# Performance work log

Hardware: AMD Instinct MI355X
Metric: run time of the kernel (lower is better)

## Reference

```python
import jax, jax.numpy as jnp
import numpy as np

CAPACITY = 0.5


def setup_inputs() -> dict:
    key = jax.random.key(0)
    ks = jax.random.split(key, 7)
    b, s, d, h = 4, 8192, 1024, 4096
    sc_r = 1.0 / np.sqrt(d)
    sc_1 = 1.0 / np.sqrt(d)
    sc_2 = 1.0 / np.sqrt(h)
    return {
        "x": jax.random.normal(ks[0], (b, s, d), dtype=jnp.float32),
        # router Linear(d, 1)
        "w_r": jax.random.uniform(ks[1], (d, 1), jnp.float32, -sc_r, sc_r),
        "b_r": jax.random.uniform(ks[2], (1,), jnp.float32, -sc_r, sc_r),
        # token-wise MLP block: Linear(d, h) -> GELU -> Linear(h, d)
        "W1": jax.random.uniform(ks[3], (d, h), jnp.float32, -sc_1, sc_1),
        "b1": jax.random.uniform(ks[4], (h,), jnp.float32, -sc_1, sc_1),
        "W2": jax.random.uniform(ks[5], (h, d), jnp.float32, -sc_2, sc_2),
        "b2": jax.random.uniform(ks[6], (d,), jnp.float32, -sc_2, sc_2),
    }


def reference(x, w_r, b_r, W1, b1, W2, b2):
    b, s, d = x.shape
    k = int(CAPACITY * s)
    # router: Linear(d,1) -> squeeze -> [b, s]
    weights = (jnp.einsum("bsd,do->bso", x, w_r) + b_r).squeeze(-1)
    # k-th largest per batch row (topk sorted descending, take last)
    top_vals, _ = jax.lax.top_k(weights, k)  # [b, k]
    threshold = top_vals[:, -1]              # [b]
    selected = weights > threshold[:, None]  # strict >, ties excluded (as in torch code)
    # token-wise block applied densely; mask-combine is exact equivalent of
    # gather -> block -> scatter for a per-token block
    hidden = jax.nn.gelu(jnp.einsum("bsd,dh->bsh", x, W1) + b1, approximate=False)
    blk = jnp.einsum("bsh,hd->bsd", hidden, W2) + b2
    m = selected[..., None]
    return jnp.where(m, blk, x)
```

## Files before the change

### kernel.cpp

```cpp
#include <hip/hip_runtime.h>

typedef unsigned short u16;
typedef __attribute__((ext_vector_type(8))) short short8;
typedef __attribute__((ext_vector_type(4))) float f32x4;

#define B_ 4
#define S_ 8192
#define D_ 1024
#define H_ 4096
#define NTOK (B_*S_)
#define MPAD 16384
#define KSEL 4096

__device__ __forceinline__ u16 f2b(float f) {
    unsigned u = __float_as_uint(f);
    unsigned r = (u + 0x7FFFu + ((u >> 16) & 1u)) >> 16;
    return (u16)r;
}

__device__ __forceinline__ void async_load16(const void* g, void* l) {
    __builtin_amdgcn_global_load_lds(
        (const __attribute__((address_space(1))) void*)g,
        (__attribute__((address_space(3))) void*)l, 16, 0, 0);
}

__global__ void init_kernel(int* __restrict__ idx, int* __restrict__ cnt) {
    int t = blockIdx.x * 256 + threadIdx.x;
    if (t < MPAD) idx[t] = 0;
    if (t == 0) *cnt = 0;
}

__global__ __launch_bounds__(256)
void router_kernel(const float* __restrict__ x, const float* __restrict__ w_r,
                   const float* __restrict__ b_r, float* __restrict__ out,
                   u16* __restrict__ xb, float* __restrict__ wts) {
    int wv = threadIdx.x >> 6, lane = threadIdx.x & 63;
    long t = (long)blockIdx.x * 4 + wv;
    const float4* xrow = (const float4*)x + t * 256;
    const float4* wr4  = (const float4*)w_r;
    float4* orow = (float4*)out + t * 256;
    double acc = 0.0;
#pragma unroll
    for (int j = 0; j < 4; ++j) {
        int e = lane + j * 64;
        float4 v = xrow[e];
        float4 w = wr4[e];
        acc += (double)v.x * w.x + (double)v.y * w.y +
               (double)v.z * w.z + (double)v.w * w.w;
        orow[e] = v;
        uint2 hv;
        hv.x = (unsigned)f2b(v.x) | ((unsigned)f2b(v.y) << 16);
        hv.y = (unsigned)f2b(v.z) | ((unsigned)f2b(v.w) << 16);
        *(uint2*)&xb[t * D_ + e * 4] = hv;
    }
#pragma unroll
    for (int off = 32; off > 0; off >>= 1) acc += __shfl_down(acc, off);
    if (lane == 0) wts[t] = (float)(acc + (double)b_r[0]);
}

__global__ void select_kernel(const float* __restrict__ w, float* __restrict__ thr) {
    int b = blockIdx.x;
    const float* wb = w + b * S_;
    __shared__ int hist[256];
    __shared__ unsigned s_prefix;
    __shared__ int s_rank;
    int tid = threadIdx.x;
    if (tid == 0) { s_prefix = 0u; s_rank = S_ - KSEL; }
    __syncthreads();
    for (int pass = 0; pass < 4; ++pass) {
        int shift = 24 - 8 * pass;
        hist[tid] = 0;
        __syncthreads();
        unsigned pfx = s_prefix;
        for (int i = tid; i < S_; i += 256) {
            unsigned u = __float_as_uint(wb[i]);
            u = (u & 0x80000000u) ? ~u : (u | 0x80000000u);
            if (pass == 0 || (u >> (shift + 8)) == pfx)
                atomicAdd(&hist[(u >> shift) & 0xFF], 1);
        }
        __syncthreads();
        if (tid == 0) {
            int r = s_rank;
            unsigned d;
            for (d = 0; d < 256; ++d) { int c = hist[d]; if (r < c) break; r -= c; }
            s_rank = r;
            s_prefix = (s_prefix << 8) | d;
        }
        __syncthreads();
    }
    if (tid == 0) {
        unsigned u = s_prefix;
        unsigned orig = (u & 0x80000000u) ? (u ^ 0x80000000u) : ~u;
        thr[b] = __uint_as_float(orig);
    }
}

__global__ void compact_kernel(const float* __restrict__ w, const float* __restrict__ thr,
                               int* __restrict__ idx, int* __restrict__ cnt) {
    int t = blockIdx.x * 256 + threadIdx.x;
    int b = t >> 13;
    if (w[t] > thr[b]) {
        int p = atomicAdd(cnt, 1);
        idx[p] = t;
    }
}

__global__ void transpose_kernel(const float* __restrict__ W, u16* __restrict__ Wt,
                                 int R, int C) {
    __shared__ float tile[32][33];
    int c0 = blockIdx.x * 32, r0 = blockIdx.y * 32;
    int tx = threadIdx.x & 31, ty = threadIdx.x >> 5;
#pragma unroll
    for (int i = 0; i < 32; i += 8)
        tile[ty + i][tx] = W[(long)(r0 + ty + i) * C + c0 + tx];
    __syncthreads();
#pragma unroll
    for (int i = 0; i < 32; i += 8)
        Wt[(long)(c0 + ty + i) * R + r0 + tx] = f2b(tile[tx][ty + i]);
}

template<int NT, int NTILES, int MODE>
__global__ __launch_bounds__(512, 2)
void gemm8p(const u16* __restrict__ A, const u16* __restrict__ Bm,
            const float* __restrict__ bias, const int* __restrict__ idx,
            const int* __restrict__ cnt, void* __restrict__ outp) {
    extern __shared__ char smem[];
    constexpr int NI = NT / 2;
    constexpr long RB = (long)NT * 128;
    constexpr int LOG_NT = (NTILES == 16) ? 4 : 2;
    const int tid = threadIdx.x;
    const int lane = tid & 63;
    const int wv = tid >> 6, wm = wv >> 2, wn = wv & 3;
    const int fr = lane & 15, fq = lane >> 4;

    constexpr int NWG = NTILES * 64;
    constexpr int QX = NWG / 8;
    const int wg = blockIdx.x + blockIdx.y * NTILES;
    const int swz = (wg & 7) * QX + (wg >> 3);
    const int ntile = swz & (NTILES - 1);
    const int mtile = swz >> LOG_NT;

    const int rl_s = tid >> 3;
    const unsigned colb = (unsigned)(((tid & 7) * 16) ^ ((rl_s & 7) << 4));
    const char* srcA[4]; const char* srcB[4];
#pragma unroll
    for (int h = 0; h < 2; ++h)
#pragma unroll
        for (int l = 0; l < 2; ++l) {
            int rl = h * 128 + l * 64 + rl_s;
            long arow = (MODE == 0) ? (long)idx[mtile * 256 + rl]
                                    : (long)(mtile * 256 + rl);
            srcA[h * 2 + l] = (const char*)A + arow * RB + colb;
            srcB[h * 2 + l] = (const char*)Bm + (long)(ntile * 256 + rl) * RB + colb;
        }
    const unsigned dstOff = (unsigned)((tid >> 3) * 128 + (tid & 7) * 16);

    const unsigned arowb = (unsigned)((wm * 128 + fr) * 128);
    const unsigned browb = (unsigned)((wn * 64 + fr) * 128);
    unsigned ck[2];
    ck[0] = (unsigned)((fq * 16) ^ ((fr & 7) << 4));
    ck[1] = ck[0] ^ 64u;

#define STAGE_A(t, h, db) { \
    async_load16(srcA[(h)*2+0] + (long)(t)*128, smem + (db)*32768 + (h)*16384 + dstOff); \
    async_load16(srcA[(h)*2+1] + (long)(t)*128, smem + (db)*32768 + (h)*16384 + 8192 + dstOff); }
#define STAGE_B(t, h, db) { \
    async_load16(srcB[(h)*2+0] + (long)(t)*128, smem + 65536 + (db)*32768 + (h)*16384 + dstOff); \
    async_load16(srcB[(h)*2+1] + (long)(t)*128, smem + 65536 + (db)*32768 + (h)*16384 + 8192 + dstOff); }
#define BAR() __builtin_amdgcn_s_barrier()
#define VM4() asm volatile("s_waitcnt vmcnt(4)" ::: "memory")

    f32x4 acc[8][4] = {};
    short8 bfr[2][4];

    STAGE_A(0, 0, 0); STAGE_A(0, 1, 0);
    STAGE_B(0, 0, 0); STAGE_B(0, 1, 0);
    STAGE_B(1, 0, 1); STAGE_B(1, 1, 1);
    asm volatile("s_waitcnt vmcnt(4)" ::: "memory");
    BAR();

#define PHASE(DB, KK, SLAB, BLOAD, STAGE_STMT) { \
    constexpr unsigned rdb = (DB) * 32768u; \
    if (BLOAD) { \
        _Pragma("unroll") \
        for (int n = 0; n < 4; ++n) \
            bfr[KK][n] = *(const short8*)(smem + (65536u + rdb + (unsigned)(n) * 2048u) + browb + ck[KK]); \
    } \
    short8 afr[4]; \
    _Pragma("unroll") \
    for (int r = 0; r < 4; ++r) \
        afr[r] = *(const short8*)(smem + (rdb + (unsigned)((SLAB) + r) * 2048u) + arowb + ck[KK]); \
    STAGE_STMT; \
    BAR(); \
    __builtin_amdgcn_s_setprio(1); \
    _Pragma("unroll") \
    for (int r = 0; r < 4; ++r) \
        _Pragma("unroll") \
        for (int n = 0; n < 4; ++n) \
            acc[(SLAB) + r][n] = __builtin_amdgcn_mfma_f32_16x16x32_bf16( \
                afr[r], bfr[KK][n], acc[(SLAB) + r][n], 0, 0, 0); \
    __builtin_amdgcn_s_setprio(0); }

    for (int i = 0; i < NI; ++i) {
        const int t0 = 2 * i;
        const int tA1 = t0 + 1;
        const int tB2 = (t0 + 2 >= NT) ? t0     : t0 + 2;
        const int tB3 = (t0 + 3 >= NT) ? t0 + 1 : t0 + 3;
        PHASE(0, 0, 0, true,  STAGE_A(tA1, 0, 1)); BAR();
        PHASE(0, 1, 0, true,  STAGE_A(tA1, 1, 1)); BAR();
        PHASE(0, 0, 4, false, STAGE_B(tB2, 0, 0)); BAR();
        PHASE(0, 1, 4, false, STAGE_B(tB2, 1, 0)); VM4(); BAR();
        PHASE(1, 0, 0, true,  STAGE_A(tB2, 0, 0)); BAR();
        PHASE(1, 1, 0, true,  STAGE_A(tB2, 1, 0)); BAR();
        PHASE(1, 0, 4, false, STAGE_B(tB3, 0, 1)); BAR();
        PHASE(1, 1, 4, false, STAGE_B(tB3, 1, 1)); VM4(); BAR();
    }
    asm volatile("s_waitcnt vmcnt(0)" ::: "memory");
    BAR();

    if constexpr (MODE == 0) {
        u16* lt = (u16*)smem;
#pragma unroll
        for (int m = 0; m < 8; ++m)
#pragma unroll
            for (int n = 0; n < 4; ++n) {
                const int lcol = wn * 64 + n * 16 + fr;
                const float bv = bias[ntile * 256 + lcol];
#pragma unroll
                for (int j = 0; j < 4; ++j) {
                    const int lrow = wm * 128 + m * 16 + fq * 4 + j;
                    float v = acc[m][n][j] + bv;
                    float z = 1.5957691216f * (v + 0.044715f * v * v * v);
                    float g = v / (1.0f + __expf(-z));
                    lt[lrow * 256 + (lcol ^ ((lrow & 7) << 3))] = f2b(g);
                }
            }
        asm volatile("s_waitcnt lgkmcnt(0)" ::: "memory");
        BAR();
        u16* hidp = (u16*)outp;
        const long gbase = (long)(mtile * 256) * H_ + ntile * 256;
#pragma unroll
        for (int it = 0; it < 16; ++it) {
            const unsigned off = (unsigned)it * 8192u + (unsigned)tid * 16u;
            const int lrow = off >> 9;
            const unsigned lcolb = off & 511u;
            short8 vv = *(const short8*)(smem + (unsigned)(lrow << 9) + (lcolb ^ ((unsigned)(lrow & 7) << 4)));
            *(short8*)((char*)hidp + (gbase + (long)lrow * H_) * 2 + lcolb) = vv;
        }
    } else {
        float* op = (float*)outp;
        const int ncnt = *cnt;
        const int orow0 = mtile * 256 + wm * 128;
        const int ocol0 = ntile * 256 + wn * 64;
#pragma unroll
        for (int m = 0; m < 8; ++m)
#pragma unroll
            for (int j = 0; j < 4; ++j) {
                const int row = orow0 + m * 16 + fq * 4 + j;
                if (row < ncnt) {
                    const long ob = (long)idx[row] * D_;
#pragma unroll
                    for (int n = 0; n < 4; ++n) {
                        const int col = ocol0 + n * 16 + fr;
                        op[ob + col] = acc[m][n][j] + bias[col];
                    }
                }
            }
    }
#undef PHASE
#undef STAGE_A
#undef STAGE_B
#undef BAR
#undef VM4
}

extern "C" void kernel_launch(void* const* d_in, const int* in_sizes, int n_in,
                              void* d_out, int out_size, void* d_ws, size_t ws_size,
                              hipStream_t stream) {
    const float* x   = (const float*)d_in[0];
    const float* w_r = (const float*)d_in[1];
    const float* b_r = (const float*)d_in[2];
    const float* W1  = (const float*)d_in[3];
    const float* b1  = (const float*)d_in[4];
    const float* W2  = (const float*)d_in[5];
    const float* b2  = (const float*)d_in[6];
    float* out = (float*)d_out;

    char* p = (char*)d_ws;
    auto alloc = [&](size_t bytes) {
        char* q = p;
        p += (bytes + 255) & ~(size_t)255;
        return q;
    };
    float* wts = (float*)alloc((size_t)NTOK * 4);
    float* thr = (float*)alloc(B_ * 4);
    int*   cnt = (int*)alloc(4);
    int*   idx = (int*)alloc((size_t)MPAD * 4);
    u16*   xb  = (u16*)alloc((size_t)NTOK * D_ * 2);
    u16*   w1t = (u16*)alloc((size_t)H_ * D_ * 2);
    u16*   w2t = (u16*)alloc((size_t)H_ * D_ * 2);
    u16*   hid = (u16*)alloc((size_t)MPAD * H_ * 2);

    auto k1 = gemm8p<16, 16, 0>;
    auto k2 = gemm8p<64, 4, 1>;
    (void)hipFuncSetAttribute((const void*)k1, hipFuncAttributeMaxDynamicSharedMemorySize, 131072);
    (void)hipFuncSetAttribute((const void*)k2, hipFuncAttributeMaxDynamicSharedMemorySize, 131072);

    init_kernel<<<MPAD / 256, 256, 0, stream>>>(idx, cnt);
    router_kernel<<<NTOK / 4, 256, 0, stream>>>(x, w_r, b_r, out, xb, wts);
    select_kernel<<<B_, 256, 0, stream>>>(wts, thr);
    compact_kernel<<<NTOK / 256, 256, 0, stream>>>(wts, thr, idx, cnt);
    transpose_kernel<<<dim3(H_ / 32, D_ / 32), 256, 0, stream>>>(W1, w1t, D_, H_);
    transpose_kernel<<<dim3(D_ / 32, H_ / 32), 256, 0, stream>>>(W2, w2t, H_, D_);
    k1<<<dim3(16, 64), 512, 131072, stream>>>(xb, w1t, b1, idx, nullptr, hid);
    k2<<<dim3(4, 64), 512, 131072, stream>>>(hid, w2t, b2, idx, cnt, out);
}
```

Measured before the change: 613.7 us.

## Use register bitwise select, add sched barrier, fold GELU exp into exp2

Replaces the histogram radix select with a per-thread register-resident bitwise binary search that counts elements above each candidate, removing shared-memory atomics. It adds a sched_barrier before the barrier in the GEMM phase macro so the compiler cannot move staging loads across it. It also folds the GELU tanh-approximation constant into an exp2f argument, which saves one multiply per element. The select kernel is small, and the sched_barrier may change how instructions interleave in the main loop.

```diff
diff --git a/kernel.cpp b/kernel.cpp
--- a/kernel.cpp
+++ b/kernel.cpp
@@ -58,39 +58,35 @@
     if (lane == 0) wts[t] = (float)(acc + (double)b_r[0]);
 }
 
-__global__ void select_kernel(const float* __restrict__ w, float* __restrict__ thr) {
+__global__ __launch_bounds__(256)
+void select_kernel(const float* __restrict__ w, float* __restrict__ thr) {
     int b = blockIdx.x;
     const float* wb = w + b * S_;
-    __shared__ int hist[256];
-    __shared__ unsigned s_prefix;
-    __shared__ int s_rank;
     int tid = threadIdx.x;
-    if (tid == 0) { s_prefix = 0u; s_rank = S_ - KSEL; }
-    __syncthreads();
-    for (int pass = 0; pass < 4; ++pass) {
-        int shift = 24 - 8 * pass;
-        hist[tid] = 0;
+    unsigned uv[32];
+#pragma unroll
+    for (int j = 0; j < 32; ++j) {
+        unsigned u = __float_as_uint(wb[tid + j * 256]);
+        uv[j] = (u & 0x80000000u) ? ~u : (u | 0x80000000u);
+    }
+    __shared__ int partial[4];
+    unsigned res = 0u;
+    for (int bit = 31; bit >= 0; --bit) {
+        unsigned cand = res | (1u << bit);
+        int c = 0;
+#pragma unroll
+        for (int j = 0; j < 32; ++j) c += (uv[j] > cand) ? 1 : 0;
+#pragma unroll
+        for (int off = 32; off > 0; off >>= 1) c += __shfl_down(c, off);
+        if ((tid & 63) == 0) partial[tid >> 6] = c;
         __syncthreads();
-        unsigned pfx = s_prefix;
-        for (int i = tid; i < S_; i += 256) {
-            unsigned u = __float_as_uint(wb[i]);
-            u = (u & 0x80000000u) ? ~u : (u | 0x80000000u);
-            if (pass == 0 || (u >> (shift + 8)) == pfx)
-                atomicAdd(&hist[(u >> shift) & 0xFF], 1);
-        }
+        int tot = partial[0] + partial[1] + partial[2] + partial[3];
+        if (tot >= KSEL) res = cand;
         __syncthreads();
-        if (tid == 0) {
-            int r = s_rank;
-            unsigned d;
-            for (d = 0; d < 256; ++d) { int c = hist[d]; if (r < c) break; r -= c; }
-            s_rank = r;
-            s_prefix = (s_prefix << 8) | d;
-        }
-        __syncthreads();
     }
     if (tid == 0) {
-        unsigned u = s_prefix;
-        unsigned orig = (u & 0x80000000u) ? (u ^ 0x80000000u) : ~u;
+        unsigned vu = res + 1u;
+        unsigned orig = (vu & 0x80000000u) ? (vu ^ 0x80000000u) : ~vu;
         thr[b] = __uint_as_float(orig);
     }
 }
@@ -191,6 +187,7 @@
     for (int r = 0; r < 4; ++r) \
         afr[r] = *(const short8*)(smem + (rdb + (unsigned)((SLAB) + r) * 2048u) + arowb + ck[KK]); \
     STAGE_STMT; \
+    __builtin_amdgcn_sched_barrier(0); \
     BAR(); \
     __builtin_amdgcn_s_setprio(1); \
     _Pragma("unroll") \
@@ -230,8 +227,8 @@
                 for (int j = 0; j < 4; ++j) {
                     const int lrow = wm * 128 + m * 16 + fq * 4 + j;
                     float v = acc[m][n][j] + bv;
-                    float z = 1.5957691216f * (v + 0.044715f * v * v * v);
-                    float g = v / (1.0f + __expf(-z));
+                    float z2 = -2.3021582f * (v + 0.044715f * v * v * v);
+                    float g = v / (1.0f + exp2f(z2));
                     lt[lrow * 256 + (lcol ^ ((lrow & 7) << 3))] = f2b(g);
                 }
             }
```

Result: faster. 580.3 us (-5.4%).
